# Optimization experiments

Hardware: AMD Instinct MI355X
Metric: run time of the kernel (lower is better)

Reference implementation:

```python
import jax, jax.numpy as jnp
import numpy as np

B, N, D = 256, 128, 512
NUM_TYPES, NUM_STATS = 6, 8
W_TYPE, W_STATS, W_CORR = 1.0, 1.0, 0.5
LN_EPS = 1e-5


def setup_inputs() -> dict:
    key = jax.random.key(0)
    ks = jax.random.split(key, 20)
    s = 1.0 / np.sqrt(D)
    inp = {
        "column_embeddings": jax.random.normal(ks[0], (B, N, D), jnp.float32),
        "masked_columns": jax.random.bernoulli(ks[1], 0.15, (B, N)),
        "type_targets": jax.random.randint(ks[2], (N,), 0, NUM_TYPES),
        "column_statistics": jax.random.normal(ks[3], (B, N, NUM_STATS), jnp.float32),
        "column_correlations": jnp.tanh(jax.random.normal(ks[4], (B, N, N), jnp.float32)),
        # type head: Linear(D,D) -> GELU -> LayerNorm -> Linear(D,NUM_TYPES)
        "t_W1": jax.random.normal(ks[5], (D, D), jnp.float32) * s,
        "t_b1": jnp.zeros((D,), jnp.float32),
        "t_g": jnp.ones((D,), jnp.float32),
        "t_beta": jnp.zeros((D,), jnp.float32),
        "t_W2": jax.random.normal(ks[6], (D, NUM_TYPES), jnp.float32) * s,
        "t_b2": jnp.zeros((NUM_TYPES,), jnp.float32),
        # stats head
        "s_W1": jax.random.normal(ks[7], (D, D), jnp.float32) * s,
        "s_b1": jnp.zeros((D,), jnp.float32),
        "s_g": jnp.ones((D,), jnp.float32),
        "s_beta": jnp.zeros((D,), jnp.float32),
        "s_W2": jax.random.normal(ks[8], (D, NUM_STATS), jnp.float32) * s,
        "s_b2": jnp.zeros((NUM_STATS,), jnp.float32),
        # bilinear correlation: x_i^T W x_j + b
        "c_W": jax.random.normal(ks[9], (D, D), jnp.float32) * s,
        "c_b": jnp.zeros((), jnp.float32),
    }
    return inp


def _mlp_head(x, W1, b1, g, beta, W2, b2):
    h = jax.nn.gelu(x @ W1 + b1, approximate=False)
    mu = h.mean(-1, keepdims=True)
    var = ((h - mu) ** 2).mean(-1, keepdims=True)
    h = (h - mu) * jax.lax.rsqrt(var + LN_EPS) * g + beta
    return h @ W2 + b2


def _forward(column_embeddings, masked_columns, type_targets,
             column_statistics, column_correlations,
             t_W1, t_b1, t_g, t_beta, t_W2, t_b2,
             s_W1, s_b1, s_g, s_beta, s_W2, s_b2,
             c_W, c_b):
    e = column_embeddings  # [B,N,D]
    type_logits = _mlp_head(e, t_W1, t_b1, t_g, t_beta, t_W2, t_b2)   # [B,N,T]
    stats_preds = _mlp_head(e, s_W1, s_b1, s_g, s_beta, s_W2, s_b2)   # [B,N,S]

    # batched bilinear correlation: tanh(e_i W e_j + b), diag forced to 1
    u = jnp.einsum('bnd,de->bne', e, c_W)            # [B,N,D]
    corr = jnp.tanh(jnp.einsum('bne,bme->bnm', u, e) + c_b)  # [B,N,N]
    eye = jnp.eye(e.shape[1], dtype=corr.dtype)
    corr = corr * (1.0 - eye) + eye

    m = masked_columns.astype(jnp.float32)           # [B,N]
    n_masked = jnp.maximum(m.sum(), 1.0)

    # type loss: masked-mean cross entropy; targets broadcast over batch
    logp = jax.nn.log_softmax(type_logits, axis=-1)
    tgt = jnp.broadcast_to(type_targets[None, :], m.shape)
    ce = -jnp.take_along_axis(logp, tgt[..., None], axis=-1)[..., 0]  # [B,N]
    type_loss = (ce * m).sum() / n_masked

    # stats loss: masked-mean MSE over [B,N,S]
    se = (stats_preds - column_statistics) ** 2
    stats_loss = (se * m[..., None]).sum() / (n_masked * se.shape[-1])

    # correlation loss: mask_expanded = m_i | m_j
    me = jnp.maximum(m[:, :, None], m[:, None, :])   # [B,N,N]
    n_me = jnp.maximum(me.sum(), 1.0)
    ce2 = (corr - column_correlations) ** 2
    correlation_loss = (ce2 * me).sum() / n_me

    total = W_TYPE * type_loss + W_STATS * stats_loss + W_CORR * correlation_loss
    return total


def reference(column_embeddings, masked_columns, type_targets,
              column_statistics, column_correlations,
              t_W1, t_b1, t_g, t_beta, t_W2, t_b2,
              s_W1, s_b1, s_g, s_beta, s_W2, s_b2,
              c_W, c_b):
    return _forward(column_embeddings, masked_columns, type_targets,
                    column_statistics, column_correlations,
                    t_W1, t_b1, t_g, t_beta, t_W2, t_b2,
                    s_W1, s_b1, s_g, s_beta, s_W2, s_b2,
                    c_W, c_b)
```

## Files before the change

### kernel.cpp

```cpp
#include <hip/hip_runtime.h>
#include <math.h>

#define Bx 256
#define Nx 128
#define Dx 512
#define Mx (Bx * Nx)
#define NTYPES 6
#define NSTATS 8
#define LN_EPS 1e-5f
#define CAP 8192

typedef __attribute__((ext_vector_type(8))) short frag8;
typedef __attribute__((ext_vector_type(4))) float f32x4;

__device__ __forceinline__ unsigned short f2bf(float f) {
    unsigned u = __float_as_uint(f);
    u += 0x7fff + ((u >> 16) & 1);
    return (unsigned short)(u >> 16);
}
__device__ __forceinline__ float bf2f(unsigned short s) {
    return __uint_as_float((unsigned)s << 16);
}

#define ASYNC16(g, l) __builtin_amdgcn_global_load_lds(                      \
    (const __attribute__((address_space(1))) void*)(g),                      \
    (__attribute__((address_space(3))) void*)(l), 16, 0, 0)

#define EB_OFF    0ULL
#define U_OFF     33554432ULL
#define HC_OFF    67108864ULL
#define WT_OFF    83886080ULL
#define WTC_OFF   84934656ULL
#define LIST_OFF  85458944ULL
#define CNTS_OFF  85590016ULL
#define PACC_OFF  85591040ULL
#define PCORR_OFF 85593088ULL
#define CNTP_OFF  85594112ULL

__global__ __launch_bounds__(256) void k_prep(
    const float* __restrict__ e, const float* __restrict__ W0,
    const float* __restrict__ W1, const float* __restrict__ W2,
    unsigned short* __restrict__ Eb, unsigned short* __restrict__ Tcmb,
    unsigned short* __restrict__ Tc, const int* __restrict__ m,
    int* __restrict__ list, int* __restrict__ cnts, int* cntp) {
    const int bid = blockIdx.x;
    const int t = threadIdx.x;
    if (bid < 256) {
        const int b = bid;
        const int r = b * Nx + t;
        int v = 0;
        if (t < 128) v = (m[r] != 0) ? 1 : 0;
        const unsigned long long bal = __ballot(v);
        const int wid = t >> 6, lane = t & 63;
        __shared__ int wcnt[2];
        __shared__ int base;
        if (lane == 0 && wid < 2) wcnt[wid] = __popcll(bal);
        __syncthreads();
        const int cnt = wcnt[0] + wcnt[1];
        if (t == 0) {
            base = atomicAdd(cntp, cnt);
            cnts[b] = cnt;
        }
        __syncthreads();
        if (t < 128 && v) {
            const int rank = __popcll(bal & ((1ULL << lane) - 1)) +
                             (wid ? wcnt[0] : 0);
            const int p = base + rank;
            if (p < CAP) list[p] = r;
        }
        return;
    }
    if (bid < 1024) {
        const int lin = (bid - 256) * 256 + t;
        const int mid = lin >> 16;
        const int i4  = (lin & 65535) * 4;
        const int n = i4 >> 9, k = i4 & 511;
        const float* W = (mid == 0) ? W0 : (mid == 1) ? W1 : W2;
        unsigned short* T = (mid == 2) ? Tc : (Tcmb + mid * 262144);
        unsigned short o[4];
#pragma unroll
        for (int j = 0; j < 4; ++j) o[j] = f2bf(W[(k + j) * Dx + n]);
        uint2 u;
        u.x = (unsigned)o[0] | ((unsigned)o[1] << 16);
        u.y = (unsigned)o[2] | ((unsigned)o[3] << 16);
        *(uint2*)(T + i4) = u;
        return;
    }
    const int r = (bid - 1024) * 4 + (t >> 6);
    const int lane = t & 63;
    const float4* src = (const float4*)(e + (size_t)r * Dx);
    const float4 a = src[lane * 2];
    const float4 b = src[lane * 2 + 1];
    unsigned short u[8] = {f2bf(a.x), f2bf(a.y), f2bf(a.z), f2bf(a.w),
                           f2bf(b.x), f2bf(b.y), f2bf(b.z), f2bf(b.w)};
    ((uint4*)(Eb + (size_t)r * Dx))[lane] = *(const uint4*)u;
}

__global__ __launch_bounds__(256) void k_gemms(
    const unsigned short* __restrict__ Eb,
    const unsigned short* __restrict__ Wtc,
    const unsigned short* __restrict__ Wtcmb,
    const float* __restrict__ bias0, const float* __restrict__ bias1,
    unsigned short* __restrict__ U, unsigned short* __restrict__ Hc,
    const int* __restrict__ list, const int* __restrict__ cntp) {
    __shared__ unsigned short As[2 * 4096];
    __shared__ unsigned short Bs[2 * 4096];
    const int bid = blockIdx.x;
    const int t = threadIdx.x;
    const unsigned short* Bt;
    unsigned short* C;
    int row0, col0, ldc, head, ra0, ra1;
    if (bid < 1024) {
        row0 = ((((bid >> 5) << 3) | (bid & 7))) << 7;
        col0 = ((bid >> 3) & 3) << 7;
        Bt = Wtc; C = U; ldc = 512; head = 0;
        ra0 = row0 + (t >> 2);
        ra1 = ra0 + 64;
    } else {
        const int b2 = bid - 1024;
        row0 = (b2 >> 3) << 7;
        const int cnt = min(*cntp, CAP);
        if (row0 >= cnt) return;
        col0 = (b2 & 7) << 7;
        Bt = Wtcmb; C = Hc; ldc = 1024; head = 1;
        ra0 = list[min(row0 + (t >> 2), cnt - 1)];
        ra1 = list[min(row0 + 64 + (t >> 2), cnt - 1)];
    }
    const int w = t >> 6, l = t & 63;
    const int wr = (w >> 1) * 64, wcol = (w & 1) * 64;
    const int quad = l >> 4, mr = l & 15;

    const unsigned short* Ag0 = Eb + (size_t)ra0 * Dx + (t & 3) * 8;
    const unsigned short* Ag1 = Eb + (size_t)ra1 * Dx + (t & 3) * 8;
    const unsigned short* Bg0 = Bt + (size_t)(col0 + (t >> 2)) * Dx + (t & 3) * 8;
    const unsigned short* Bg1 = Bg0 + (size_t)64 * Dx;

    f32x4 acc[4][4] = {};
    for (int k0 = 0; k0 < Dx; k0 += 64) {
        __syncthreads();
#pragma unroll
        for (int s = 0; s < 2; ++s) {
            ASYNC16(Ag0 + k0 + s * 32, As + s * 4096 + t * 8);
            ASYNC16(Ag1 + k0 + s * 32, As + s * 4096 + (t + 256) * 8);
            ASYNC16(Bg0 + k0 + s * 32, Bs + s * 4096 + t * 8);
            ASYNC16(Bg1 + k0 + s * 32, Bs + s * 4096 + (t + 256) * 8);
        }
        __syncthreads();
#pragma unroll
        for (int s = 0; s < 2; ++s) {
            frag8 a[4], b[4];
#pragma unroll
            for (int i = 0; i < 4; ++i)
                a[i] = *(const frag8*)&As[s * 4096 + (wr + i * 16 + mr) * 32 + quad * 8];
#pragma unroll
            for (int j = 0; j < 4; ++j)
                b[j] = *(const frag8*)&Bs[s * 4096 + (wcol + j * 16 + mr) * 32 + quad * 8];
#pragma unroll
            for (int i = 0; i < 4; ++i)
#pragma unroll
                for (int j = 0; j < 4; ++j)
                    acc[i][j] = __builtin_amdgcn_mfma_f32_16x16x32_bf16(
                        a[i], b[j], acc[i][j], 0, 0, 0);
        }
    }
#pragma unroll
    for (int i = 0; i < 4; ++i)
#pragma unroll
        for (int j = 0; j < 4; ++j)
#pragma unroll
            for (int r = 0; r < 4; ++r) {
                const int row = row0 + wr + i * 16 + quad * 4 + r;
                const int col = col0 + wcol + j * 16 + mr;
                float v = acc[i][j][r];
                if (head) {
                    v += (col < 512) ? bias0[col] : bias1[col - 512];
                    v = 0.5f * v * (1.0f + erff(v * 0.70710678118654752f));
                }
                C[(size_t)row * ldc + col] = f2bf(v);
            }
}

__global__ __launch_bounds__(256) void k_tail(
    const unsigned short* __restrict__ U,
    const unsigned short* __restrict__ Eb,
    const float* __restrict__ Ct, const int* __restrict__ m,
    const float* __restrict__ cbp, float* __restrict__ pcorr,
    const unsigned short* __restrict__ Hc,
    const float* __restrict__ tg, const float* __restrict__ tbeta,
    const float* __restrict__ tW2, const float* __restrict__ tb2,
    const float* __restrict__ sg, const float* __restrict__ sbeta,
    const float* __restrict__ sW2, const float* __restrict__ sb2,
    const int* __restrict__ list, const int* __restrict__ cntp,
    const int* __restrict__ tgt, const float* __restrict__ stats,
    float* __restrict__ pacc) {
    __shared__ unsigned short As[2 * 4096];
    __shared__ unsigned short Bs[2 * 4096];
    __shared__ float mloc[128];
    __shared__ float redf[4][2];
    const int t = threadIdx.x;
    const int w = t >> 6, l = t & 63;

    if (blockIdx.x < 256) {
        const int b = blockIdx.x;
        const int wr = (w >> 1) * 64, wcol = (w & 1) * 64;
        const int quad = l >> 4, mr = l & 15;
        if (t < 128) mloc[t] = (m[b * Nx + t] != 0) ? 1.0f : 0.0f;

        const unsigned short* Ub = U + (size_t)b * Nx * Dx;
        const unsigned short* E  = Eb + (size_t)b * Nx * Dx;
        const unsigned short* Ag0 = Ub + (size_t)(t >> 2) * Dx + (t & 3) * 8;
        const unsigned short* Ag1 = Ag0 + (size_t)64 * Dx;
        const unsigned short* Bg0 = E + (size_t)(t >> 2) * Dx + (t & 3) * 8;
        const unsigned short* Bg1 = Bg0 + (size_t)64 * Dx;

        f32x4 acc_r[4][4] = {};
        for (int k0 = 0; k0 < Dx; k0 += 64) {
            __syncthreads();
#pragma unroll
            for (int s = 0; s < 2; ++s) {
                ASYNC16(Ag0 + k0 + s * 32, As + s * 4096 + t * 8);
                ASYNC16(Ag1 + k0 + s * 32, As + s * 4096 + (t + 256) * 8);
                ASYNC16(Bg0 + k0 + s * 32, Bs + s * 4096 + t * 8);
                ASYNC16(Bg1 + k0 + s * 32, Bs + s * 4096 + (t + 256) * 8);
            }
            __syncthreads();
#pragma unroll
            for (int s = 0; s < 2; ++s) {
                frag8 a[4], bfr[4];
#pragma unroll
                for (int i = 0; i < 4; ++i)
                    a[i] = *(const frag8*)&As[s * 4096 + (wr + i * 16 + mr) * 32 + quad * 8];
#pragma unroll
                for (int j = 0; j < 4; ++j)
                    bfr[j] = *(const frag8*)&Bs[s * 4096 + (wcol + j * 16 + mr) * 32 + quad * 8];
#pragma unroll
                for (int i = 0; i < 4; ++i)
#pragma unroll
                    for (int j = 0; j < 4; ++j)
                        acc_r[i][j] = __builtin_amdgcn_mfma_f32_16x16x32_bf16(
                            a[i], bfr[j], acc_r[i][j], 0, 0, 0);
            }
        }
        const float cb = cbp[0];
        float lsum = 0.0f;
#pragma unroll
        for (int i = 0; i < 4; ++i)
#pragma unroll
            for (int j = 0; j < 4; ++j)
#pragma unroll
                for (int r = 0; r < 4; ++r) {
                    const int row = wr + i * 16 + quad * 4 + r;
                    const int col = wcol + j * 16 + mr;
                    float c = (row == col) ? 1.0f : tanhf(acc_r[i][j][r] + cb);
                    const float me = fmaxf(mloc[row], mloc[col]);
                    const float d = c - Ct[((size_t)b * Nx + row) * Nx + col];
                    lsum += me * d * d;
                }
#pragma unroll
        for (int off = 32; off > 0; off >>= 1) lsum += __shfl_down(lsum, off);
        if (l == 0) redf[w][0] = lsum;
        __syncthreads();
        if (t == 0) pcorr[b] = redf[0][0] + redf[1][0] + redf[2][0] + redf[3][0];
        return;
    }

    const int blk = blockIdx.x - 256;
    const int cnt = min(*cntp, CAP);
    float ce_acc = 0.0f, sse_acc = 0.0f;
    for (int idx = blk * 4 + w; idx < cnt; idx += 256 * 4) {
        const int r = list[idx];
        const uint4 ut = ((const uint4*)(Hc + (size_t)idx * 1024))[l];
        const uint4 us = ((const uint4*)(Hc + (size_t)idx * 1024 + 512))[l];
        float a[8], b8[8];
        {
            const unsigned uu[4] = {ut.x, ut.y, ut.z, ut.w};
            const unsigned vv[4] = {us.x, us.y, us.z, us.w};
#pragma unroll
            for (int j = 0; j < 4; ++j) {
                a[2 * j]      = bf2f((unsigned short)(uu[j] & 0xffff));
                a[2 * j + 1]  = bf2f((unsigned short)(uu[j] >> 16));
                b8[2 * j]     = bf2f((unsigned short)(vv[j] & 0xffff));
                b8[2 * j + 1] = bf2f((unsigned short)(vv[j] >> 16));
            }
        }
        float st = 0, qt = 0, ss = 0, qs = 0;
#pragma unroll
        for (int j = 0; j < 8; ++j) {
            st += a[j]; qt += a[j] * a[j];
            ss += b8[j]; qs += b8[j] * b8[j];
        }
#pragma unroll
        for (int off = 32; off > 0; off >>= 1) {
            st += __shfl_xor(st, off); qt += __shfl_xor(qt, off);
            ss += __shfl_xor(ss, off); qs += __shfl_xor(qs, off);
        }
        const float mt = st * (1.0f / Dx);
        const float rt = rsqrtf(qt * (1.0f / Dx) - mt * mt + LN_EPS);
        const float ms = ss * (1.0f / Dx);
        const float rs = rsqrtf(qs * (1.0f / Dx) - ms * ms + LN_EPS);

        const int c0 = l * 8;
        float tp[6] = {}, sp[8] = {};
#pragma unroll
        for (int j = 0; j < 8; ++j) {
            const int c = c0 + j;
            const float nt = (a[j] - mt) * rt * tg[c] + tbeta[c];
#pragma unroll
            for (int k = 0; k < 6; ++k) tp[k] += nt * tW2[c * 6 + k];
            const float ns = (b8[j] - ms) * rs * sg[c] + sbeta[c];
#pragma unroll
            for (int k = 0; k < 8; ++k) sp[k] += ns * sW2[c * 8 + k];
        }
#pragma unroll
        for (int k = 0; k < 6; ++k)
#pragma unroll
            for (int off = 32; off > 0; off >>= 1) tp[k] += __shfl_down(tp[k], off);
#pragma unroll
        for (int k = 0; k < 8; ++k)
#pragma unroll
            for (int off = 32; off > 0; off >>= 1) sp[k] += __shfl_down(sp[k], off);

        if (l == 0) {
            float lg[6];
#pragma unroll
            for (int k = 0; k < 6; ++k) lg[k] = tp[k] + tb2[k];
            float mx = lg[0];
#pragma unroll
            for (int k = 1; k < 6; ++k) mx = fmaxf(mx, lg[k]);
            float se = 0.0f;
#pragma unroll
            for (int k = 0; k < 6; ++k) se += expf(lg[k] - mx);
            ce_acc += -(lg[tgt[r & (Nx - 1)]] - mx - logf(se));
            float sse = 0.0f;
#pragma unroll
            for (int k = 0; k < 8; ++k) {
                const float d = sp[k] + sb2[k] - stats[(size_t)r * NSTATS + k];
                sse += d * d;
            }
            sse_acc += sse;
        }
    }
    if (l == 0) { redf[w][0] = ce_acc; redf[w][1] = sse_acc; }
    __syncthreads();
    if (t == 0) {
        pacc[2 * blk]     = redf[0][0] + redf[1][0] + redf[2][0] + redf[3][0];
        pacc[2 * blk + 1] = redf[0][1] + redf[1][1] + redf[2][1] + redf[3][1];
    }
}

__global__ __launch_bounds__(256) void k_final(
    const float* __restrict__ pacc, const float* __restrict__ pcorr,
    const int* __restrict__ cnts, const int* __restrict__ cntp,
    float* __restrict__ out) {
    const int t = threadIdx.x, w = t >> 6, lane = t & 63;
    float ce = pacc[2 * t], sse = pacc[2 * t + 1], co = pcorr[t];
    const int c = cnts[t];
    float me = (float)(Nx * Nx) - (float)((Nx - c) * (Nx - c));
#pragma unroll
    for (int off = 32; off > 0; off >>= 1) {
        ce += __shfl_down(ce, off);
        sse += __shfl_down(sse, off);
        co += __shfl_down(co, off);
        me += __shfl_down(me, off);
    }
    __shared__ float red[4][4];
    if (lane == 0) {
        red[w][0] = ce; red[w][1] = sse; red[w][2] = co; red[w][3] = me;
    }
    __syncthreads();
    if (t == 0) {
        const float CE = red[0][0] + red[1][0] + red[2][0] + red[3][0];
        const float SSE = red[0][1] + red[1][1] + red[2][1] + red[3][1];
        const float CO = red[0][2] + red[1][2] + red[2][2] + red[3][2];
        const float ME = red[0][3] + red[1][3] + red[2][3] + red[3][3];
        const float nm = fmaxf((float)*cntp, 1.0f);
        const float nme = fmaxf(ME, 1.0f);
        out[0] = CE / nm + SSE / (nm * (float)NSTATS) + 0.5f * CO / nme;
    }
}

extern "C" void kernel_launch(void* const* d_in, const int* in_sizes, int n_in,
                              void* d_out, int out_size, void* d_ws, size_t ws_size,
                              hipStream_t stream) {
    const float* e      = (const float*)d_in[0];
    const int*   mcols  = (const int*)d_in[1];
    const int*   ttgt   = (const int*)d_in[2];
    const float* stats  = (const float*)d_in[3];
    const float* corrT  = (const float*)d_in[4];
    const float* tW1    = (const float*)d_in[5];
    const float* tb1    = (const float*)d_in[6];
    const float* tg     = (const float*)d_in[7];
    const float* tbeta  = (const float*)d_in[8];
    const float* tW2    = (const float*)d_in[9];
    const float* tb2    = (const float*)d_in[10];
    const float* sW1    = (const float*)d_in[11];
    const float* sb1    = (const float*)d_in[12];
    const float* sg     = (const float*)d_in[13];
    const float* sbeta  = (const float*)d_in[14];
    const float* sW2    = (const float*)d_in[15];
    const float* sb2    = (const float*)d_in[16];
    const float* cW     = (const float*)d_in[17];
    const float* cb     = (const float*)d_in[18];
    float* out = (float*)d_out;

    char* ws = (char*)d_ws;
    unsigned short* Eb    = (unsigned short*)(ws + EB_OFF);
    unsigned short* U     = (unsigned short*)(ws + U_OFF);
    unsigned short* Hc    = (unsigned short*)(ws + HC_OFF);
    unsigned short* Wtcmb = (unsigned short*)(ws + WT_OFF);
    unsigned short* Wtc   = (unsigned short*)(ws + WTC_OFF);
    int*   list  = (int*)(ws + LIST_OFF);
    int*   cnts  = (int*)(ws + CNTS_OFF);
    float* pacc  = (float*)(ws + PACC_OFF);
    float* pcorr = (float*)(ws + PCORR_OFF);
    int*   cntp  = (int*)(ws + CNTP_OFF);

    hipMemsetAsync(cntp, 0, sizeof(int), stream);
    k_prep<<<9216, 256, 0, stream>>>(e, tW1, sW1, cW, Eb, Wtcmb, Wtc, mcols,
                                     list, cnts, cntp);
    k_gemms<<<1536, 256, 0, stream>>>(Eb, Wtc, Wtcmb, tb1, sb1, U, Hc, list, cntp);
    k_tail<<<512, 256, 0, stream>>>(U, Eb, corrT, mcols, cb, pcorr,
                                    Hc, tg, tbeta, tW2, tb2, sg, sbeta, sW2, sb2,
                                    list, cntp, ttgt, stats, pacc);
    k_final<<<1, 256, 0, stream>>>(pacc, pcorr, cnts, cntp, out);
}
```

Before: 239.5 us.

## Restrict bilinear correlation to masked rows and fuse GEMMs with pipelined loads

The correlation loss only needs entries where row or column is masked, so the bilinear GEMM is now computed only for masked columns (U = E_m W and V = E_m W^T) instead of the full [B,N,N] product for every row. This removes the dense U GEMM over all rows. The projection GEMM now uses 256-wide tiles, a double-buffered async pipeline with XOR-swizzled LDS and raised priority during MFMA, and weight transposes go through shared-memory tiles. The final reduction kernel is replaced by atomics plus a last-block-done finalize. The cost is more complex per-batch index bookkeeping, variable tile counts, and float atomic ordering nondeterminism.

```diff
diff --git a/kernel.cpp b/kernel.cpp
--- a/kernel.cpp
+++ b/kernel.cpp
@@ -4,7 +4,6 @@
 #define Bx 256
 #define Nx 128
 #define Dx 512
-#define Mx (Bx * Nx)
 #define NTYPES 6
 #define NSTATS 8
 #define LN_EPS 1e-5f
@@ -26,23 +25,30 @@
     (const __attribute__((address_space(1))) void*)(g),                      \
     (__attribute__((address_space(3))) void*)(l), 16, 0, 0)
 
+#define VWAIT(NIMM)                                                          \
+    asm volatile("s_waitcnt vmcnt(" #NIMM ")" ::: "memory");                 \
+    __builtin_amdgcn_sched_barrier(0);
+#define BARX __builtin_amdgcn_s_barrier();
+
 #define EB_OFF    0ULL
-#define U_OFF     33554432ULL
-#define HC_OFF    67108864ULL
-#define WT_OFF    83886080ULL
-#define WTC_OFF   84934656ULL
-#define LIST_OFF  85458944ULL
-#define CNTS_OFF  85590016ULL
-#define PACC_OFF  85591040ULL
-#define PCORR_OFF 85593088ULL
-#define CNTP_OFF  85594112ULL
+#define HC_OFF    33554432ULL
+#define WT_OFF    67108864ULL
+#define WTC_OFF   68157440ULL
+#define WC_OFF    68681728ULL
+#define LIST_OFF  69206016ULL
+#define CNTS_OFF  69238784ULL
+#define BASES_OFF 69239808ULL
+#define CNTP_OFF  69240832ULL
+#define ACC_OFF   69240848ULL
+#define DONE_OFF  69240864ULL
 
 __global__ __launch_bounds__(256) void k_prep(
     const float* __restrict__ e, const float* __restrict__ W0,
     const float* __restrict__ W1, const float* __restrict__ W2,
     unsigned short* __restrict__ Eb, unsigned short* __restrict__ Tcmb,
-    unsigned short* __restrict__ Tc, const int* __restrict__ m,
-    int* __restrict__ list, int* __restrict__ cnts, int* cntp) {
+    unsigned short* __restrict__ Tc, unsigned short* __restrict__ Wc,
+    const int* __restrict__ m, int* __restrict__ list,
+    int* __restrict__ cnts, int* __restrict__ bases, int* cntp) {
     const int bid = blockIdx.x;
     const int t = threadIdx.x;
     if (bid < 256) {
@@ -60,6 +66,7 @@
         if (t == 0) {
             base = atomicAdd(cntp, cnt);
             cnts[b] = cnt;
+            bases[b] = base;
         }
         __syncthreads();
         if (t < 128 && v) {
@@ -70,23 +77,44 @@
         }
         return;
     }
-    if (bid < 1024) {
-        const int lin = (bid - 256) * 256 + t;
-        const int mid = lin >> 16;
-        const int i4  = (lin & 65535) * 4;
-        const int n = i4 >> 9, k = i4 & 511;
+    if (bid < 448) {
+        const int lin = bid - 256;
+        const int mid = lin >> 6;
+        const int tl  = lin & 63;
+        const int ti = tl >> 3, tj = tl & 7;
         const float* W = (mid == 0) ? W0 : (mid == 1) ? W1 : W2;
         unsigned short* T = (mid == 2) ? Tc : (Tcmb + mid * 262144);
-        unsigned short o[4];
-#pragma unroll
-        for (int j = 0; j < 4; ++j) o[j] = f2bf(W[(k + j) * Dx + n]);
-        uint2 u;
-        u.x = (unsigned)o[0] | ((unsigned)o[1] << 16);
-        u.y = (unsigned)o[2] | ((unsigned)o[3] << 16);
-        *(uint2*)(T + i4) = u;
+        __shared__ float sh[64][65];
+        const int c = t & 63;
+        const int r4 = t >> 6;
+#pragma unroll
+        for (int rr = 0; rr < 16; ++rr) {
+            const int row = rr * 4 + r4;
+            sh[row][c] = W[(size_t)(ti * 64 + row) * Dx + tj * 64 + c];
+        }
+        __syncthreads();
+#pragma unroll
+        for (int rr = 0; rr < 16; ++rr) {
+            const int col2 = rr * 4 + r4;
+            T[(size_t)(tj * 64 + col2) * Dx + ti * 64 + c] = f2bf(sh[c][col2]);
+        }
         return;
     }
-    const int r = (bid - 1024) * 4 + (t >> 6);
+    if (bid < 512) {
+        const int base = (bid - 448) * 4096 + t * 16;
+        const float4* src = (const float4*)(W2 + base);
+        unsigned short o[16];
+#pragma unroll
+        for (int q = 0; q < 4; ++q) {
+            const float4 v = src[q];
+            o[q * 4 + 0] = f2bf(v.x); o[q * 4 + 1] = f2bf(v.y);
+            o[q * 4 + 2] = f2bf(v.z); o[q * 4 + 3] = f2bf(v.w);
+        }
+        *(uint4*)(Wc + base) = *(const uint4*)(o);
+        *(uint4*)(Wc + base + 8) = *(const uint4*)(o + 8);
+        return;
+    }
+    const int r = (bid - 512) * 4 + (t >> 6);
     const int lane = t & 63;
     const float4* src = (const float4*)(e + (size_t)r * Dx);
     const float4 a = src[lane * 2];
@@ -96,72 +124,67 @@
     ((uint4*)(Eb + (size_t)r * Dx))[lane] = *(const uint4*)u;
 }
 
-__global__ __launch_bounds__(256) void k_gemms(
+__global__ __launch_bounds__(512) void k_gemms(
     const unsigned short* __restrict__ Eb,
+    const unsigned short* __restrict__ Wtcmb,
     const unsigned short* __restrict__ Wtc,
-    const unsigned short* __restrict__ Wtcmb,
+    const unsigned short* __restrict__ Wc,
     const float* __restrict__ bias0, const float* __restrict__ bias1,
-    unsigned short* __restrict__ U, unsigned short* __restrict__ Hc,
+    unsigned short* __restrict__ Hc,
     const int* __restrict__ list, const int* __restrict__ cntp) {
     __shared__ unsigned short As[2 * 4096];
-    __shared__ unsigned short Bs[2 * 4096];
+    __shared__ unsigned short Bs[2 * 8192];
     const int bid = blockIdx.x;
     const int t = threadIdx.x;
-    const unsigned short* Bt;
-    unsigned short* C;
-    int row0, col0, ldc, head, ra0, ra1;
-    if (bid < 1024) {
-        row0 = ((((bid >> 5) << 3) | (bid & 7))) << 7;
-        col0 = ((bid >> 3) & 3) << 7;
-        Bt = Wtc; C = U; ldc = 512; head = 0;
-        ra0 = row0 + (t >> 2);
-        ra1 = ra0 + 64;
-    } else {
-        const int b2 = bid - 1024;
-        row0 = (b2 >> 3) << 7;
-        const int cnt = min(*cntp, CAP);
-        if (row0 >= cnt) return;
-        col0 = (b2 & 7) << 7;
-        Bt = Wtcmb; C = Hc; ldc = 1024; head = 1;
-        ra0 = list[min(row0 + (t >> 2), cnt - 1)];
-        ra1 = list[min(row0 + 64 + (t >> 2), cnt - 1)];
-    }
+    const int cnt = min(*cntp, CAP);
+    const int rt = ((bid >> 6) << 3) | (bid & 7);
+    const int row0 = rt << 7;
+    if (row0 >= cnt) return;
+    const int ct = (bid >> 3) & 7;
+    const int col0 = ct << 8;
+    const unsigned short* Bbase =
+        (ct < 4) ? (Wtcmb + (size_t)ct * 256 * Dx)
+      : (ct < 6) ? (Wtc + (size_t)(ct - 4) * 256 * Dx)
+                 : (Wc + (size_t)(ct - 6) * 256 * Dx);
+    const int kq = (t & 3) ^ ((t >> 3) & 3);
+    const int ra = list[min(row0 + (t >> 2), cnt - 1)];
+    const unsigned short* pA = Eb + (size_t)ra * Dx + kq * 8;
+    const unsigned short* pB0 = Bbase + (size_t)(t >> 2) * Dx + kq * 8;
+    const unsigned short* pB1 = pB0 + (size_t)128 * Dx;
     const int w = t >> 6, l = t & 63;
-    const int wr = (w >> 1) * 64, wcol = (w & 1) * 64;
+    const int wr = (w >> 2) * 64, wcol = (w & 3) * 64;
     const int quad = l >> 4, mr = l & 15;
-
-    const unsigned short* Ag0 = Eb + (size_t)ra0 * Dx + (t & 3) * 8;
-    const unsigned short* Ag1 = Eb + (size_t)ra1 * Dx + (t & 3) * 8;
-    const unsigned short* Bg0 = Bt + (size_t)(col0 + (t >> 2)) * Dx + (t & 3) * 8;
-    const unsigned short* Bg1 = Bg0 + (size_t)64 * Dx;
+    const int co = (quad ^ ((mr >> 1) & 3)) * 8;
+
+#define MSTAGE(bf, k0)                                                       \
+  { ASYNC16(pA + (k0), As + (bf) * 4096 + t * 8);                            \
+    ASYNC16(pB0 + (k0), Bs + (bf) * 8192 + t * 8);                           \
+    ASYNC16(pB1 + (k0), Bs + (bf) * 8192 + 4096 + t * 8); }
 
     f32x4 acc[4][4] = {};
-    for (int k0 = 0; k0 < Dx; k0 += 64) {
-        __syncthreads();
-#pragma unroll
-        for (int s = 0; s < 2; ++s) {
-            ASYNC16(Ag0 + k0 + s * 32, As + s * 4096 + t * 8);
-            ASYNC16(Ag1 + k0 + s * 32, As + s * 4096 + (t + 256) * 8);
-            ASYNC16(Bg0 + k0 + s * 32, Bs + s * 4096 + t * 8);
-            ASYNC16(Bg1 + k0 + s * 32, Bs + s * 4096 + (t + 256) * 8);
-        }
-        __syncthreads();
-#pragma unroll
-        for (int s = 0; s < 2; ++s) {
-            frag8 a[4], b[4];
-#pragma unroll
-            for (int i = 0; i < 4; ++i)
-                a[i] = *(const frag8*)&As[s * 4096 + (wr + i * 16 + mr) * 32 + quad * 8];
+    MSTAGE(0, 0);
+    int buf = 0;
+    for (int k = 0; k < 16; ++k) {
+        if (k < 15) { MSTAGE(buf ^ 1, (k + 1) * 32); VWAIT(3); }
+        else        { VWAIT(0); }
+        BARX;
+        frag8 af[4], bfv[4];
+#pragma unroll
+        for (int i = 0; i < 4; ++i)
+            af[i] = *(const frag8*)&As[buf * 4096 + (wr + i * 16 + mr) * 32 + co];
+#pragma unroll
+        for (int j = 0; j < 4; ++j)
+            bfv[j] = *(const frag8*)&Bs[buf * 8192 + (wcol + j * 16 + mr) * 32 + co];
+        __builtin_amdgcn_s_setprio(1);
+#pragma unroll
+        for (int i = 0; i < 4; ++i)
 #pragma unroll
             for (int j = 0; j < 4; ++j)
-                b[j] = *(const frag8*)&Bs[s * 4096 + (wcol + j * 16 + mr) * 32 + quad * 8];
-#pragma unroll
-            for (int i = 0; i < 4; ++i)
-#pragma unroll
-                for (int j = 0; j < 4; ++j)
-                    acc[i][j] = __builtin_amdgcn_mfma_f32_16x16x32_bf16(
-                        a[i], b[j], acc[i][j], 0, 0, 0);
-        }
+                acc[i][j] = __builtin_amdgcn_mfma_f32_16x16x32_bf16(
+                    af[i], bfv[j], acc[i][j], 0, 0, 0);
+        __builtin_amdgcn_s_setprio(0);
+        if (k < 15) BARX;
+        buf ^= 1;
     }
 #pragma unroll
     for (int i = 0; i < 4; ++i)
@@ -172,210 +195,261 @@
                 const int row = row0 + wr + i * 16 + quad * 4 + r;
                 const int col = col0 + wcol + j * 16 + mr;
                 float v = acc[i][j][r];
-                if (head) {
+                if (col < 1024) {
                     v += (col < 512) ? bias0[col] : bias1[col - 512];
                     v = 0.5f * v * (1.0f + erff(v * 0.70710678118654752f));
                 }
-                C[(size_t)row * ldc + col] = f2bf(v);
-            }
+                Hc[(size_t)row * 2048 + col] = f2bf(v);
+            }
+#undef MSTAGE
 }
 
 __global__ __launch_bounds__(256) void k_tail(
-    const unsigned short* __restrict__ U,
     const unsigned short* __restrict__ Eb,
     const float* __restrict__ Ct, const int* __restrict__ m,
-    const float* __restrict__ cbp, float* __restrict__ pcorr,
+    const float* __restrict__ cbp,
     const unsigned short* __restrict__ Hc,
     const float* __restrict__ tg, const float* __restrict__ tbeta,
     const float* __restrict__ tW2, const float* __restrict__ tb2,
     const float* __restrict__ sg, const float* __restrict__ sbeta,
     const float* __restrict__ sW2, const float* __restrict__ sb2,
-    const int* __restrict__ list, const int* __restrict__ cntp,
+    const int* __restrict__ list, const int* __restrict__ cnts,
+    const int* __restrict__ bases, const int* __restrict__ cntp,
     const int* __restrict__ tgt, const float* __restrict__ stats,
-    float* __restrict__ pacc) {
-    __shared__ unsigned short As[2 * 4096];
-    __shared__ unsigned short Bs[2 * 4096];
+    float* __restrict__ accs, int* __restrict__ done,
+    float* __restrict__ out) {
+    __shared__ unsigned short Elds[2 * 4096];
+    __shared__ unsigned short Ulds[2 * 4096];
+    __shared__ unsigned short Vlds[2 * 4096];
     __shared__ float mloc[128];
+    __shared__ int lrow[128];
     __shared__ float redf[4][2];
     const int t = threadIdx.x;
     const int w = t >> 6, l = t & 63;
+    const int quad = l >> 4, mr = l & 15;
 
     if (blockIdx.x < 256) {
         const int b = blockIdx.x;
-        const int wr = (w >> 1) * 64, wcol = (w & 1) * 64;
-        const int quad = l >> 4, mr = l & 15;
-        if (t < 128) mloc[t] = (m[b * Nx + t] != 0) ? 1.0f : 0.0f;
-
-        const unsigned short* Ub = U + (size_t)b * Nx * Dx;
-        const unsigned short* E  = Eb + (size_t)b * Nx * Dx;
-        const unsigned short* Ag0 = Ub + (size_t)(t >> 2) * Dx + (t & 3) * 8;
-        const unsigned short* Ag1 = Ag0 + (size_t)64 * Dx;
-        const unsigned short* Bg0 = E + (size_t)(t >> 2) * Dx + (t & 3) * 8;
-        const unsigned short* Bg1 = Bg0 + (size_t)64 * Dx;
-
-        f32x4 acc_r[4][4] = {};
-        for (int k0 = 0; k0 < Dx; k0 += 64) {
-            __syncthreads();
-#pragma unroll
-            for (int s = 0; s < 2; ++s) {
-                ASYNC16(Ag0 + k0 + s * 32, As + s * 4096 + t * 8);
-                ASYNC16(Ag1 + k0 + s * 32, As + s * 4096 + (t + 256) * 8);
-                ASYNC16(Bg0 + k0 + s * 32, Bs + s * 4096 + t * 8);
-                ASYNC16(Bg1 + k0 + s * 32, Bs + s * 4096 + (t + 256) * 8);
-            }
-            __syncthreads();
-#pragma unroll
-            for (int s = 0; s < 2; ++s) {
-                frag8 a[4], bfr[4];
-#pragma unroll
-                for (int i = 0; i < 4; ++i)
-                    a[i] = *(const frag8*)&As[s * 4096 + (wr + i * 16 + mr) * 32 + quad * 8];
-#pragma unroll
-                for (int j = 0; j < 4; ++j)
-                    bfr[j] = *(const frag8*)&Bs[s * 4096 + (wcol + j * 16 + mr) * 32 + quad * 8];
-#pragma unroll
-                for (int i = 0; i < 4; ++i)
-#pragma unroll
-                    for (int j = 0; j < 4; ++j)
-                        acc_r[i][j] = __builtin_amdgcn_mfma_f32_16x16x32_bf16(
-                            a[i], bfr[j], acc_r[i][j], 0, 0, 0);
-            }
-        }
-        const float cb = cbp[0];
-        float lsum = 0.0f;
-#pragma unroll
-        for (int i = 0; i < 4; ++i)
-#pragma unroll
-            for (int j = 0; j < 4; ++j)
-#pragma unroll
-                for (int r = 0; r < 4; ++r) {
-                    const int row = wr + i * 16 + quad * 4 + r;
-                    const int col = wcol + j * 16 + mr;
-                    float c = (row == col) ? 1.0f : tanhf(acc_r[i][j][r] + cb);
-                    const float me = fmaxf(mloc[row], mloc[col]);
-                    const float d = c - Ct[((size_t)b * Nx + row) * Nx + col];
-                    lsum += me * d * d;
+        const int cnt = cnts[b];
+        const int cbase = bases[b];
+        const int nt = (cnt + 15) >> 4;
+        if (t < 128) {
+            mloc[t] = (m[b * Nx + t] != 0) ? 1.0f : 0.0f;
+            lrow[t] = (t < cnt) ? (list[cbase + t] & (Nx - 1)) : 0;
+        }
+        __syncthreads();
+        float T1 = 0.0f, T2 = 0.0f, Tov = 0.0f;
+        if (cnt > 0) {
+            const int kq = (t & 3) ^ ((t >> 3) & 3);
+            const size_t rb = (size_t)b * Nx;
+            const unsigned short* pE0 = Eb + (rb + (t >> 2)) * Dx + kq * 8;
+            const unsigned short* pE1 = Eb + (rb + 64 + (t >> 2)) * Dx + kq * 8;
+            const int ur0 = min((t >> 2), cnt - 1);
+            const int ur1 = min(64 + (t >> 2), cnt - 1);
+            const unsigned short* pU0 = Hc + (size_t)(cbase + ur0) * 2048 + 1024 + kq * 8;
+            const unsigned short* pU1 = Hc + (size_t)(cbase + ur1) * 2048 + 1024 + kq * 8;
+            const unsigned short* pV0 = Hc + (size_t)(cbase + ur0) * 2048 + 1536 + kq * 8;
+            const unsigned short* pV1 = Hc + (size_t)(cbase + ur1) * 2048 + 1536 + kq * 8;
+            const int co = (quad ^ ((mr >> 1) & 3)) * 8;
+
+#define CSTAGE(bf, k0)                                                       \
+  { ASYNC16(pE0 + (k0), Elds + (bf) * 4096 + t * 8);                         \
+    ASYNC16(pE1 + (k0), Elds + (bf) * 4096 + 2048 + t * 8);                  \
+    ASYNC16(pU0 + (k0), Ulds + (bf) * 4096 + t * 8);                         \
+    ASYNC16(pU1 + (k0), Ulds + (bf) * 4096 + 2048 + t * 8);                  \
+    ASYNC16(pV0 + (k0), Vlds + (bf) * 4096 + t * 8);                         \
+    ASYNC16(pV1 + (k0), Vlds + (bf) * 4096 + 2048 + t * 8); }
+
+            f32x4 ar[8][2] = {};
+            f32x4 ac[2][8] = {};
+            CSTAGE(0, 0);
+            int buf = 0;
+            for (int k = 0; k < 16; ++k) {
+                if (k < 15) { CSTAGE(buf ^ 1, (k + 1) * 32); VWAIT(6); }
+                else        { VWAIT(0); }
+                BARX;
+                frag8 ef[2];
+#pragma unroll
+                for (int eidx = 0; eidx < 2; ++eidx)
+                    ef[eidx] = *(const frag8*)&Elds[buf * 4096 +
+                        (w * 32 + eidx * 16 + mr) * 32 + co];
+                __builtin_amdgcn_s_setprio(1);
+#pragma unroll
+                for (int it = 0; it < 8; ++it)
+                    if (it < nt) {
+                        const frag8 uf = *(const frag8*)&Ulds[buf * 4096 +
+                            (it * 16 + mr) * 32 + co];
+                        ar[it][0] = __builtin_amdgcn_mfma_f32_16x16x32_bf16(
+                            uf, ef[0], ar[it][0], 0, 0, 0);
+                        ar[it][1] = __builtin_amdgcn_mfma_f32_16x16x32_bf16(
+                            uf, ef[1], ar[it][1], 0, 0, 0);
+                    }
+#pragma unroll
+                for (int jt = 0; jt < 8; ++jt)
+                    if (jt < nt) {
+                        const frag8 vf = *(const frag8*)&Vlds[buf * 4096 +
+                            (jt * 16 + mr) * 32 + co];
+                        ac[0][jt] = __builtin_amdgcn_mfma_f32_16x16x32_bf16(
+                            ef[0], vf, ac[0][jt], 0, 0, 0);
+                        ac[1][jt] = __builtin_amdgcn_mfma_f32_16x16x32_bf16(
+                            ef[1], vf, ac[1][jt], 0, 0, 0);
+                    }
+                __builtin_amdgcn_s_setprio(0);
+                if (k < 15) BARX;
+                buf ^= 1;
+            }
+            const float cb = cbp[0];
+            const float* Ctb = Ct + (size_t)b * Nx * Nx;
+#pragma unroll
+            for (int it = 0; it < 8; ++it)
+                if (it < nt) {
+#pragma unroll
+                    for (int eidx = 0; eidx < 2; ++eidx) {
+                        const int j = w * 32 + eidx * 16 + mr;
+#pragma unroll
+                        for (int r = 0; r < 4; ++r) {
+                            const int pos = it * 16 + quad * 4 + r;
+                            if (pos < cnt) {
+                                const int i = lrow[pos];
+                                const float s = ar[it][eidx][r];
+                                const float c = (i == j) ? 1.0f : tanhf(s + cb);
+                                const float d = c - Ctb[i * Nx + j];
+                                T1 += d * d;
+                                Tov += d * d * mloc[j];
+                            }
+                        }
+                    }
                 }
+#pragma unroll
+            for (int jt = 0; jt < 8; ++jt)
+                if (jt < nt) {
+                    const int pos = jt * 16 + mr;
+                    const int valid = (pos < cnt);
+                    const int j = lrow[pos];
+#pragma unroll
+                    for (int eidx = 0; eidx < 2; ++eidx) {
+#pragma unroll
+                        for (int r = 0; r < 4; ++r) {
+                            if (valid) {
+                                const int i = w * 32 + eidx * 16 + quad * 4 + r;
+                                const float s = ac[eidx][jt][r];
+                                const float c = (i == j) ? 1.0f : tanhf(s + cb);
+                                const float d = c - Ctb[i * Nx + j];
+                                T2 += d * d;
+                            }
+                        }
+                    }
+                }
+#undef CSTAGE
+        }
+        float lsum = T1 + T2 - Tov;
 #pragma unroll
         for (int off = 32; off > 0; off >>= 1) lsum += __shfl_down(lsum, off);
         if (l == 0) redf[w][0] = lsum;
         __syncthreads();
-        if (t == 0) pcorr[b] = redf[0][0] + redf[1][0] + redf[2][0] + redf[3][0];
-        return;
-    }
-
-    const int blk = blockIdx.x - 256;
-    const int cnt = min(*cntp, CAP);
-    float ce_acc = 0.0f, sse_acc = 0.0f;
-    for (int idx = blk * 4 + w; idx < cnt; idx += 256 * 4) {
-        const int r = list[idx];
-        const uint4 ut = ((const uint4*)(Hc + (size_t)idx * 1024))[l];
-        const uint4 us = ((const uint4*)(Hc + (size_t)idx * 1024 + 512))[l];
-        float a[8], b8[8];
-        {
-            const unsigned uu[4] = {ut.x, ut.y, ut.z, ut.w};
-            const unsigned vv[4] = {us.x, us.y, us.z, us.w};
-#pragma unroll
-            for (int j = 0; j < 4; ++j) {
-                a[2 * j]      = bf2f((unsigned short)(uu[j] & 0xffff));
-                a[2 * j + 1]  = bf2f((unsigned short)(uu[j] >> 16));
-                b8[2 * j]     = bf2f((unsigned short)(vv[j] & 0xffff));
-                b8[2 * j + 1] = bf2f((unsigned short)(vv[j] >> 16));
-            }
-        }
-        float st = 0, qt = 0, ss = 0, qs = 0;
-#pragma unroll
-        for (int j = 0; j < 8; ++j) {
-            st += a[j]; qt += a[j] * a[j];
-            ss += b8[j]; qs += b8[j] * b8[j];
-        }
-#pragma unroll
-        for (int off = 32; off > 0; off >>= 1) {
-            st += __shfl_xor(st, off); qt += __shfl_xor(qt, off);
-            ss += __shfl_xor(ss, off); qs += __shfl_xor(qs, off);
-        }
-        const float mt = st * (1.0f / Dx);
-        const float rt = rsqrtf(qt * (1.0f / Dx) - mt * mt + LN_EPS);
-        const float ms = ss * (1.0f / Dx);
-        const float rs = rsqrtf(qs * (1.0f / Dx) - ms * ms + LN_EPS);
-
-        const int c0 = l * 8;
-        float tp[6] = {}, sp[8] = {};
-#pragma unroll
-        for (int j = 0; j < 8; ++j) {
-            const int c = c0 + j;
-            const float nt = (a[j] - mt) * rt * tg[c] + tbeta[c];
-#pragma unroll
-            for (int k = 0; k < 6; ++k) tp[k] += nt * tW2[c * 6 + k];
-            const float ns = (b8[j] - ms) * rs * sg[c] + sbeta[c];
-#pragma unroll
-            for (int k = 0; k < 8; ++k) sp[k] += ns * sW2[c * 8 + k];
-        }
-#pragma unroll
-        for (int k = 0; k < 6; ++k)
-#pragma unroll
-            for (int off = 32; off > 0; off >>= 1) tp[k] += __shfl_down(tp[k], off);
-#pragma unroll
-        for (int k = 0; k < 8; ++k)
-#pragma unroll
-            for (int off = 32; off > 0; off >>= 1) sp[k] += __shfl_down(sp[k], off);
-
-        if (l == 0) {
-            float lg[6];
-#pragma unroll
-            for (int k = 0; k < 6; ++k) lg[k] = tp[k] + tb2[k];
-            float mx = lg[0];
-#pragma unroll
-            for (int k = 1; k < 6; ++k) mx = fmaxf(mx, lg[k]);
-            float se = 0.0f;
-#pragma unroll
-            for (int k = 0; k < 6; ++k) se += expf(lg[k] - mx);
-            ce_acc += -(lg[tgt[r & (Nx - 1)]] - mx - logf(se));
-            float sse = 0.0f;
-#pragma unroll
-            for (int k = 0; k < 8; ++k) {
-                const float d = sp[k] + sb2[k] - stats[(size_t)r * NSTATS + k];
-                sse += d * d;
-            }
-            sse_acc += sse;
-        }
-    }
-    if (l == 0) { redf[w][0] = ce_acc; redf[w][1] = sse_acc; }
-    __syncthreads();
-    if (t == 0) {
-        pacc[2 * blk]     = redf[0][0] + redf[1][0] + redf[2][0] + redf[3][0];
-        pacc[2 * blk + 1] = redf[0][1] + redf[1][1] + redf[2][1] + redf[3][1];
-    }
-}
-
-__global__ __launch_bounds__(256) void k_final(
-    const float* __restrict__ pacc, const float* __restrict__ pcorr,
-    const int* __restrict__ cnts, const int* __restrict__ cntp,
-    float* __restrict__ out) {
-    const int t = threadIdx.x, w = t >> 6, lane = t & 63;
-    float ce = pacc[2 * t], sse = pacc[2 * t + 1], co = pcorr[t];
-    const int c = cnts[t];
-    float me = (float)(Nx * Nx) - (float)((Nx - c) * (Nx - c));
-#pragma unroll
-    for (int off = 32; off > 0; off >>= 1) {
-        ce += __shfl_down(ce, off);
-        sse += __shfl_down(sse, off);
-        co += __shfl_down(co, off);
-        me += __shfl_down(me, off);
-    }
-    __shared__ float red[4][4];
-    if (lane == 0) {
-        red[w][0] = ce; red[w][1] = sse; red[w][2] = co; red[w][3] = me;
+        if (t == 0) {
+            atomicAdd(&accs[2], redf[0][0] + redf[1][0] + redf[2][0] + redf[3][0]);
+            const float c = (float)cnt;
+            atomicAdd(&accs[3], 256.0f * c - c * c);
+        }
+    } else {
+        const int blk = blockIdx.x - 256;
+        const int cnt = min(*cntp, CAP);
+        float ce_acc = 0.0f, sse_acc = 0.0f;
+        for (int idx = blk * 4 + w; idx < cnt; idx += 256 * 4) {
+            const int r = list[idx];
+            const uint4 ut = ((const uint4*)(Hc + (size_t)idx * 2048))[l];
+            const uint4 us = ((const uint4*)(Hc + (size_t)idx * 2048 + 512))[l];
+            float a[8], b8[8];
+            {
+                const unsigned uu[4] = {ut.x, ut.y, ut.z, ut.w};
+                const unsigned vv[4] = {us.x, us.y, us.z, us.w};
+#pragma unroll
+                for (int j = 0; j < 4; ++j) {
+                    a[2 * j]      = bf2f((unsigned short)(uu[j] & 0xffff));
+                    a[2 * j + 1]  = bf2f((unsigned short)(uu[j] >> 16));
+                    b8[2 * j]     = bf2f((unsigned short)(vv[j] & 0xffff));
+                    b8[2 * j + 1] = bf2f((unsigned short)(vv[j] >> 16));
+                }
+            }
+            float st = 0, qt = 0, ss = 0, qs = 0;
+#pragma unroll
+            for (int j = 0; j < 8; ++j) {
+                st += a[j]; qt += a[j] * a[j];
+                ss += b8[j]; qs += b8[j] * b8[j];
+            }
+#pragma unroll
+            for (int off = 32; off > 0; off >>= 1) {
+                st += __shfl_xor(st, off); qt += __shfl_xor(qt, off);
+                ss += __shfl_xor(ss, off); qs += __shfl_xor(qs, off);
+            }
+            const float mt = st * (1.0f / Dx);
+            const float rt = rsqrtf(qt * (1.0f / Dx) - mt * mt + LN_EPS);
+            const float ms = ss * (1.0f / Dx);
+            const float rs = rsqrtf(qs * (1.0f / Dx) - ms * ms + LN_EPS);
+
+            const int c0 = l * 8;
+            float tp[6] = {}, sp[8] = {};
+#pragma unroll
+            for (int j = 0; j < 8; ++j) {
+                const int c = c0 + j;
+                const float nt2 = (a[j] - mt) * rt * tg[c] + tbeta[c];
+#pragma unroll
+                for (int k = 0; k < 6; ++k) tp[k] += nt2 * tW2[c * 6 + k];
+                const float ns = (b8[j] - ms) * rs * sg[c] + sbeta[c];
+#pragma unroll
+                for (int k = 0; k < 8; ++k) sp[k] += ns * sW2[c * 8 + k];
+            }
+#pragma unroll
+            for (int k = 0; k < 6; ++k)
+#pragma unroll
+                for (int off = 32; off > 0; off >>= 1) tp[k] += __shfl_down(tp[k], off);
+#pragma unroll
+            for (int k = 0; k < 8; ++k)
+#pragma unroll
+                for (int off = 32; off > 0; off >>= 1) sp[k] += __shfl_down(sp[k], off);
+
+            if (l == 0) {
+                float lg[6];
+#pragma unroll
+                for (int k = 0; k < 6; ++k) lg[k] = tp[k] + tb2[k];
+                float mx = lg[0];
+#pragma unroll
+                for (int k = 1; k < 6; ++k) mx = fmaxf(mx, lg[k]);
+                float se = 0.0f;
+#pragma unroll
+                for (int k = 0; k < 6; ++k) se += expf(lg[k] - mx);
+                ce_acc += -(lg[tgt[r & (Nx - 1)]] - mx - logf(se));
+                float sse = 0.0f;
+#pragma unroll
+                for (int k = 0; k < 8; ++k) {
+                    const float d = sp[k] + sb2[k] - stats[(size_t)r * NSTATS + k];
+                    sse += d * d;
+                }
+                sse_acc += sse;
+            }
+        }
+        if (l == 0) { redf[w][0] = ce_acc; redf[w][1] = sse_acc; }
+        __syncthreads();
+        if (t == 0) {
+            atomicAdd(&accs[0], redf[0][0] + redf[1][0] + redf[2][0] + redf[3][0]);
+            atomicAdd(&accs[1], redf[0][1] + redf[1][1] + redf[2][1] + redf[3][1]);
+        }
     }
     __syncthreads();
     if (t == 0) {
-        const float CE = red[0][0] + red[1][0] + red[2][0] + red[3][0];
-        const float SSE = red[0][1] + red[1][1] + red[2][1] + red[3][1];
-        const float CO = red[0][2] + red[1][2] + red[2][2] + red[3][2];
-        const float ME = red[0][3] + red[1][3] + red[2][3] + red[3][3];
-        const float nm = fmaxf((float)*cntp, 1.0f);
-        const float nme = fmaxf(ME, 1.0f);
-        out[0] = CE / nm + SSE / (nm * (float)NSTATS) + 0.5f * CO / nme;
+        __threadfence();
+        const int old = atomicAdd(done, 1);
+        if (old == 511) {
+            __threadfence();
+            const float CE  = atomicAdd(&accs[0], 0.0f);
+            const float SSE = atomicAdd(&accs[1], 0.0f);
+            const float CO  = atomicAdd(&accs[2], 0.0f);
+            const float ME  = atomicAdd(&accs[3], 0.0f);
+            const float nm = fmaxf((float)min(*cntp, CAP), 1.0f);
+            out[0] = CE / nm + SSE / (nm * (float)NSTATS) +
+                     0.5f * CO / fmaxf(ME, 1.0f);
+        }
     }
 }
 
@@ -405,22 +479,24 @@
 
     char* ws = (char*)d_ws;
     unsigned short* Eb    = (unsigned short*)(ws + EB_OFF);
-    unsigned short* U     = (unsigned short*)(ws + U_OFF);
     unsigned short* Hc    = (unsigned short*)(ws + HC_OFF);
     unsigned short* Wtcmb = (unsigned short*)(ws + WT_OFF);
     unsigned short* Wtc   = (unsigned short*)(ws + WTC_OFF);
+    unsigned short* Wc    = (unsigned short*)(ws + WC_OFF);
     int*   list  = (int*)(ws + LIST_OFF);
     int*   cnts  = (int*)(ws + CNTS_OFF);
-    float* pacc  = (float*)(ws + PACC_OFF);
-    float* pcorr = (float*)(ws + PCORR_OFF);
+    int*   bases = (int*)(ws + BASES_OFF);
     int*   cntp  = (int*)(ws + CNTP_OFF);
-
-    hipMemsetAsync(cntp, 0, sizeof(int), stream);
-    k_prep<<<9216, 256, 0, stream>>>(e, tW1, sW1, cW, Eb, Wtcmb, Wtc, mcols,
-                                     list, cnts, cntp);
-    k_gemms<<<1536, 256, 0, stream>>>(Eb, Wtc, Wtcmb, tb1, sb1, U, Hc, list, cntp);
-    k_tail<<<512, 256, 0, stream>>>(U, Eb, corrT, mcols, cb, pcorr,
-                                    Hc, tg, tbeta, tW2, tb2, sg, sbeta, sW2, sb2,
-                                    list, cntp, ttgt, stats, pacc);
-    k_final<<<1, 256, 0, stream>>>(pacc, pcorr, cnts, cntp, out);
+    float* accs  = (float*)(ws + ACC_OFF);
+    int*   done  = (int*)(ws + DONE_OFF);
+
+    hipMemsetAsync(ws + CNTP_OFF, 0, 48, stream);
+    k_prep<<<8704, 256, 0, stream>>>(e, tW1, sW1, cW, Eb, Wtcmb, Wtc, Wc,
+                                     mcols, list, cnts, bases, cntp);
+    k_gemms<<<512, 512, 0, stream>>>(Eb, Wtcmb, Wtc, Wc, tb1, sb1, Hc,
+                                     list, cntp);
+    k_tail<<<512, 256, 0, stream>>>(Eb, corrT, mcols, cb, Hc,
+                                    tg, tbeta, tW2, tb2, sg, sbeta, sW2, sb2,
+                                    list, cnts, bases, cntp, ttgt, stats,
+                                    accs, done, out);
 }
```

Result: no change. 238.8 us (-0.3%).
